# Performance work log

Measured on AMD Instinct MI355X. Metric: run time of the kernel, lower is better.

The kernel has to match this reference:

```python
import jax, jax.numpy as jnp
import numpy as np

NEG = jnp.float32(-1e30)  # safe stand-in for -inf in log-space

def setup_inputs() -> dict:
    key = jax.random.key(0)
    k1, k2, k3, k4 = jax.random.split(key, 4)
    N, C, T, S = 64, 64, 4000, 100
    logits = jax.random.normal(k1, (N, C, T), dtype=jnp.float32)
    targets = jax.random.randint(k2, (N, S), 1, C)          # labels, no blank
    target_lengths = jax.random.randint(k3, (N,), 1, S + 1)  # >= 1
    input_lengths = jax.random.randint(k4, (N,), 2000, T + 1)
    return {"logits": logits, "targets": targets,
            "target_lengths": target_lengths, "input_lengths": input_lengths}

def _lse2(a, b):
    m = jnp.maximum(a, b)
    return m + jnp.log(jnp.exp(a - m) + jnp.exp(b - m))

def _lse3(a, b, c):
    m = jnp.maximum(jnp.maximum(a, b), c)
    return m + jnp.log(jnp.exp(a - m) + jnp.exp(b - m) + jnp.exp(c - m))

def reference(logits, targets, target_lengths, input_lengths):
    # logits: (N, C, T); blank = 0; reduction = 'mean' (per-sample / target_len, then mean)
    N, C, T = logits.shape
    S = targets.shape[1]
    L = 2 * S + 1
    lp = jax.nn.log_softmax(logits, axis=1)      # (N, C, T)
    lp = jnp.transpose(lp, (2, 0, 1))            # (T, N, C)

    # extended label sequence: blank, t1, blank, t2, ..., blank  -> (N, L)
    ext = jnp.zeros((N, L), dtype=targets.dtype).at[:, 1::2].set(targets)
    # skip transition s-2 -> s allowed iff ext[s] != blank and ext[s] != ext[s-2]
    prev2 = jnp.pad(ext[:, :-2], ((0, 0), (2, 0)), constant_values=0)
    skip_ok = (ext != 0) & (ext != prev2)        # (N, L)

    # per-time log-probs of extended labels: (T, N, L)
    lp_ext = jnp.take_along_axis(lp, jnp.broadcast_to(ext[None], (T, N, L)), axis=2)

    # alpha init at t=0
    alpha = jnp.full((N, L), NEG, dtype=lp.dtype)
    alpha = alpha.at[:, 0].set(lp_ext[0, :, 0])
    alpha = alpha.at[:, 1].set(lp_ext[0, :, 1])

    neg1 = jnp.full((N, 1), NEG, dtype=lp.dtype)
    neg2 = jnp.full((N, 2), NEG, dtype=lp.dtype)

    def step(a, inp):
        lpt, t = inp                              # lpt: (N, L)
        a1 = a
        a2 = jnp.concatenate([neg1, a[:, :-1]], axis=1)
        a3 = jnp.concatenate([neg2, a[:, :-2]], axis=1)
        a3 = jnp.where(skip_ok, a3, NEG)
        new = _lse3(a1, a2, a3) + lpt
        active = (t < input_lengths)[:, None]     # freeze past input length
        return jnp.where(active, new, a), None

    alpha, _ = jax.lax.scan(step, alpha, (lp_ext[1:], jnp.arange(1, T)))

    i1 = (2 * target_lengths)[:, None]            # last blank
    i2 = jnp.maximum(i1 - 1, 0)                   # last label
    v1 = jnp.take_along_axis(alpha, i1, axis=1)[:, 0]
    v2 = jnp.take_along_axis(alpha, i2, axis=1)[:, 0]
    loss_n = -_lse2(v1, v2)                       # (N,)
    return jnp.mean(loss_n / target_lengths.astype(loss_n.dtype))
```

## Files before the change

kernel.cpp:

```cpp
#include <hip/hip_runtime.h>
#include <cstdint>
#include <cstddef>

#define NEGV (-1e30f)
#define IL2f 1.44269504088896340736f
#define LN2f 0.693147180559945309417f

__device__ __forceinline__ float exp2_hw(float x) { return __builtin_amdgcn_exp2f(x); }
__device__ __forceinline__ float log2_hw(float x) { return __builtin_amdgcn_logf(x); }

constexpr int Nn = 64, Cc = 64, Tt = 4000, Ss = 100;

__device__ __forceinline__ float wave_shr1(float x) {
    return __int_as_float(__builtin_amdgcn_update_dpp(0, __float_as_int(x), 0x138, 0xF, 0xF, true));
}
__device__ __forceinline__ float wave_shl1(float x) {
    return __int_as_float(__builtin_amdgcn_update_dpp(0, __float_as_int(x), 0x130, 0xF, 0xF, true));
}
__device__ __forceinline__ int wave_shr1_i(int x) {
    return __builtin_amdgcn_update_dpp(0, x, 0x138, 0xF, 0xF, true);
}
__device__ __forceinline__ int wave_shl1_i(int x) {
    return __builtin_amdgcn_update_dpp(0, x, 0x130, 0xF, 0xF, true);
}

typedef float f4 __attribute__((ext_vector_type(4)));
typedef float f2 __attribute__((ext_vector_type(2)));
#define LD4(p) (*(const f4*)(p))

__device__ __forceinline__ void gload16(const float* g, float* l) {
    __builtin_amdgcn_global_load_lds(
        (const __attribute__((address_space(1))) void*)g,
        (__attribute__((address_space(3))) void*)l, 16, 0, 0);
}

__global__ __launch_bounds__(256) void ctc_denom_part(
    const float* __restrict__ logits, float* __restrict__ dP)
{
    const int t4 = (blockIdx.x * 256 + threadIdx.x) * 4;
    const int n = blockIdx.y;
    const int c0 = blockIdx.z * 32;
    if (t4 >= Tt) return;
    const float* __restrict__ p = logits + ((size_t)(n * Cc + c0)) * Tt + t4;
    f4 m, s;
    {
        f4 v = LD4(p);
        #pragma unroll
        for (int i = 0; i < 4; ++i) { m[i] = v[i] * IL2f; s[i] = 1.f; }
    }
    #pragma unroll 4
    for (int c = 1; c < 32; ++c) {
        f4 v = LD4(p + (size_t)c * Tt);
        #pragma unroll
        for (int i = 0; i < 4; ++i) {
            float vi = v[i] * IL2f;
            float nm = fmaxf(m[i], vi);
            s[i] = s[i] * exp2_hw(m[i] - nm) + exp2_hw(vi - nm);
            m[i] = nm;
        }
    }
    f4 o;
    #pragma unroll
    for (int i = 0; i < 4; ++i) o[i] = m[i] + log2_hw(s[i]);
    *(f4*)(dP + ((size_t)blockIdx.z * Nn + n) * Tt + t4) = o;
}

__global__ __launch_bounds__(256) void ctc_denom_kernel(
    const float* __restrict__ logits, float* __restrict__ d2)
{
    const int t4 = (blockIdx.x * 256 + threadIdx.x) * 4;
    const int n = blockIdx.y;
    if (t4 >= Tt) return;
    const float* __restrict__ p = logits + (size_t)n * Cc * Tt + t4;
    f4 m, s;
    {
        f4 v = LD4(p);
        #pragma unroll
        for (int i = 0; i < 4; ++i) { m[i] = v[i] * IL2f; s[i] = 1.f; }
    }
    #pragma unroll 4
    for (int c = 1; c < Cc; ++c) {
        f4 v = LD4(p + (size_t)c * Tt);
        #pragma unroll
        for (int i = 0; i < 4; ++i) {
            float vi = v[i] * IL2f;
            float nm = fmaxf(m[i], vi);
            s[i] = s[i] * exp2_hw(m[i] - nm) + exp2_hw(vi - nm);
            m[i] = nm;
        }
    }
    f4 o;
    #pragma unroll
    for (int i = 0; i < 4; ++i) o[i] = m[i] + log2_hw(s[i]);
    *(f4*)(d2 + (size_t)n * Tt + t4) = o;
}

__global__ __launch_bounds__(256) void ctc_denom_merge(float* __restrict__ dP)
{
    const int t4 = (blockIdx.x * 256 + threadIdx.x) * 4;
    const int n = blockIdx.y;
    if (t4 >= Tt) return;
    f4 a = LD4(dP + (size_t)n * Tt + t4);
    f4 b = LD4(dP + ((size_t)Nn + n) * Tt + t4);
    f4 d;
    #pragma unroll
    for (int i = 0; i < 4; ++i) {
        const float mm = fmaxf(a[i], b[i]);
        d[i] = mm + log2_hw(exp2_hw(a[i] - mm) + exp2_hw(b[i] - mm));
    }
    *(f4*)(dP + (size_t)n * Tt + t4) = d;
}

template<bool MERGE>
__global__ __launch_bounds__(256) void ctc_prob_sel(
    const float* __restrict__ logits, const float* __restrict__ dP,
    const int* __restrict__ targets, const int* __restrict__ tlen,
    float* __restrict__ P)
{
    const int n = blockIdx.y;
    const int c0 = blockIdx.z * 8;
    __shared__ int needs;
    if (threadIdx.x == 0) needs = (c0 == 0) ? 1 : 0;
    __syncthreads();
    const int tl = tlen[n];
    if ((int)threadIdx.x < min(tl, Ss)) {
        const int rel = targets[n * Ss + threadIdx.x] - c0;
        if (rel >= 0 && rel < 8) atomicOr(&needs, 1 << rel);
    }
    __syncthreads();
    const int nd = needs;
    if (nd == 0) return;
    const int t4 = (blockIdx.x * 256 + threadIdx.x) * 4;
    if (t4 >= Tt) return;
    f4 d;
    if constexpr (MERGE) {
        f4 a = LD4(dP + (size_t)n * Tt + t4);
        f4 b = LD4(dP + ((size_t)Nn + n) * Tt + t4);
        #pragma unroll
        for (int i = 0; i < 4; ++i) {
            const float mm = fmaxf(a[i], b[i]);
            d[i] = mm + log2_hw(exp2_hw(a[i] - mm) + exp2_hw(b[i] - mm));
        }
    } else {
        d = LD4(dP + (size_t)n * Tt + t4);
    }
    const float* __restrict__ src = logits + ((size_t)(n * Cc + c0)) * Tt + t4;
    float* __restrict__ dst = P + ((size_t)(n * Cc + c0)) * Tt + t4;
    #pragma unroll
    for (int c = 0; c < 8; ++c) {
        if ((nd >> c) & 1) {
            f4 v = LD4(src + (size_t)c * Tt);
            f4 o;
            #pragma unroll
            for (int i = 0; i < 4; ++i) o[i] = exp2_hw(fmaf(v[i], IL2f, -d[i]));
            *(f4*)(dst + (size_t)c * Tt) = o;
        }
    }
}

template<bool PRE>
__global__ __launch_bounds__(64) void ctc_fb_kernel(
    const float* __restrict__ PR, const int* __restrict__ targets,
    const int* __restrict__ tlen, const int* __restrict__ ilen,
    const float* __restrict__ d2, float* __restrict__ wsA, float* __restrict__ wsB)
{
    constexpr int NA = PRE ? 3 : 4;
    constexpr int NLD = NA * 8;
    __shared__ float lds[2][NA][8][64][4];

    const int bid = blockIdx.x;
    const int n = bid >> 1;
    const bool bwd = bid & 1;
    const int lane = threadIdx.x;
    const int tl = tlen[n];
    const int Tn = ilen[n];
    const int L = 2 * tl + 1;
    const int mid = Tn >> 1;
    const int s0 = 4 * lane;

    const int j1 = min(2 * lane, Ss - 1);
    const int j3 = min(2 * lane + 1, Ss - 1);
    const int base = n * Ss;
    const int tg1 = targets[base + j1];
    const int tg3 = targets[base + j3];
    const int tg1m = targets[base + max(2 * lane - 1, 0)];
    const int tg3p = targets[base + min(2 * lane + 2, Ss - 1)];

    const float sk1f = ((s0 + 1 >= 3) && (tg1 != tg1m)) ? 1.f : 0.f;
    const float sk3f = (tg3 != tg1) ? 1.f : 0.f;
    const float sk1b = ((s0 + 3 < L) && (tg3 != tg1)) ? 1.f : 0.f;
    const float sk3b = ((s0 + 5 < L) && (tg3p != tg3)) ? 1.f : 0.f;

    const float* __restrict__ rB = PR + (size_t)(n * Cc) * Tt;
    const float* __restrict__ r1 = PR + (size_t)(n * Cc + tg1) * Tt;
    const float* __restrict__ r3 = PR + (size_t)(n * Cc + tg3) * Tt;
    const float* __restrict__ rD = d2 + (size_t)n * Tt;

    float a0, a1, a2, a3;
    int E = 0;

    if (!bwd) {
        float pB0, p10;
        if constexpr (PRE) { pB0 = rB[0]; p10 = r1[0]; }
        else {
            const float dv = rD[0];
            pB0 = exp2_hw(fmaf(rB[0], IL2f, -dv));
            p10 = exp2_hw(fmaf(r1[0], IL2f, -dv));
        }
        a0 = (lane == 0) ? pB0 : 0.f;
        a1 = (lane == 0) ? p10 : 0.f;
        a2 = 0.f; a3 = 0.f;
    } else {
        const int te = Tn - 1;
        float pBe, p1e, p3e;
        if constexpr (PRE) { pBe = rB[te]; p1e = r1[te]; p3e = r3[te]; }
        else {
            const float dv = rD[te];
            pBe = exp2_hw(fmaf(rB[te], IL2f, -dv));
            p1e = exp2_hw(fmaf(r1[te], IL2f, -dv));
            p3e = exp2_hw(fmaf(r3[te], IL2f, -dv));
        }
        const int sl = 2 * tl;
        a0 = (s0 == sl) ? pBe : 0.f;
        a1 = (s0 + 1 == sl - 1) ? p1e : 0.f;
        a2 = (s0 + 2 == sl) ? pBe : 0.f;
        a3 = (s0 + 3 == sl - 1) ? p3e : 0.f;
    }

    #define ISSUE(gg, sl) {                                                         \
        const int bo_ = (gg) * 32;                                                  \
        _Pragma("unroll")                                                           \
        for (int j = 0; j < 8; ++j) {                                               \
            gload16(rB + bo_ + 4 * j, &lds[sl][0][j][0][0]);                        \
            gload16(r1 + bo_ + 4 * j, &lds[sl][1][j][0][0]);                        \
            gload16(r3 + bo_ + 4 * j, &lds[sl][2][j][0][0]);                        \
            if constexpr (!PRE) gload16(rD + bo_ + 4 * j, &lds[sl][NA - 1][j][0][0]); \
        }                                                                           \
    }
    #define WAITG() asm volatile("s_waitcnt vmcnt(%0)" :: "n"(NLD) : "memory")
    #define LOADREGS(slc)                                                           \
        f4 vB[8], vU[8], vW[8], vD[8];                                              \
        _Pragma("unroll")                                                           \
        for (int j = 0; j < 8; ++j) {                                               \
            vB[j] = LD4(&lds[slc][0][j][lane][0]);                                  \
            vU[j] = LD4(&lds[slc][1][j][lane][0]);                                  \
            vW[j] = LD4(&lds[slc][2][j][lane][0]);                                  \
            if constexpr (!PRE) vD[j] = LD4(&lds[slc][NA - 1][j][lane][0]);         \
        }                                                                           \
        (void)vD;

    #define RENORM_S(nb) {                                                          \
        const float mx = fmaxf(fmaxf(a0, a1), fmaxf(a2, a3));                       \
        const int me = (int)(__float_as_uint(mx) >> 23);                            \
        const float s2 = __int_as_float((unsigned)(254 - me) << 23);                \
        a0 *= s2; a1 *= s2; a2 *= s2; a3 *= s2;                                     \
        E = (mx > 0.f) ? (E + me - 127) : (nb);                                     \
    }

    if (!bwd) {
        const int tB = mid;
        const int gHi = tB >> 5;

        #define BODY_F_G(gg) {                                                      \
            _Pragma("unroll")                                                       \
            for (int w = 0; w < 4; ++w) {                                           \
                const int Eu = wave_shr1_i(E);                                      \
                const int eb = min(max(127 + (Eu - E), 0), 230);                    \
                const float sc = __int_as_float((unsigned)eb << 23);                \
                const float sk1fs = sk1f * sc;                                      \
                _Pragma("unroll")                                                   \
                for (int kk = 0; kk < 8; ++kk) {                                    \
                    const int k = w * 8 + kk;                                       \
                    const int t = (gg) * 32 + k;                                    \
                    if (t >= 1 && t <= tB) {                                        \
                        float pB, p1, p3;                                           \
                        if constexpr (PRE) {                                        \
                            pB = vB[k >> 2][k & 3]; p1 = vU[k >> 2][k & 3];         \
                            p3 = vW[k >> 2][k & 3];                                 \
                        } else {                                                    \
                            const float dv = vD[k >> 2][k & 3];                     \
                            pB = exp2_hw(fmaf(vB[k >> 2][k & 3], IL2f, -dv));       \
                            p1 = exp2_hw(fmaf(vU[k >> 2][k & 3], IL2f, -dv));       \
                            p3 = exp2_hw(fmaf(vW[k >> 2][k & 3], IL2f, -dv));       \
                        }                                                           \
                        const float u3 = wave_shr1(a3);                             \
                        const float n3 = fmaf(a1, sk3f, a3 + a2) * p3;              \
                        const float n2 = (a2 + a1) * pB;                            \
                        const float n1 = fmaf(u3, sk1fs, a1 + a0) * p1;             \
                        const float n0 = fmaf(u3, sc, a0) * pB;                     \
                        a0 = n0; a1 = n1; a2 = n2; a3 = n3;                         \
                    }                                                               \
                }                                                                   \
                RENORM_S(Eu);                                                       \
            }                                                                       \
        }

        #define BODY_F_F() {                                                        \
            f2 Q0 = {a0, a2}, Q1 = {a1, a3};                                        \
            _Pragma("unroll")                                                       \
            for (int w = 0; w < 4; ++w) {                                           \
                const int Eu = wave_shr1_i(E);                                      \
                const int eb = min(max(127 + (Eu - E), 0), 230);                    \
                const float sc = __int_as_float((unsigned)eb << 23);                \
                const f2 Ksk = {sk3f, sk1f * sc};                                   \
                const f2 K1s = {1.0f, sc};                                          \
                _Pragma("unroll")                                                   \
                for (int kk = 0; kk < 8; ++kk) {                                    \
                    const int k = w * 8 + kk;                                       \
                    const float pB = vB[k >> 2][k & 3];                             \
                    const f2 P31 = {vW[k >> 2][k & 3], vU[k >> 2][k & 3]};          \
                    const f2 PBB = {pB, pB};                                        \
                    const float u3 = wave_shr1(Q1.y);                               \
                    const f2 M = {Q1.x, u3};                                        \
                    const f2 Q0s = __builtin_shufflevector(Q0, Q0, 1, 0);           \
                    const f2 S = __builtin_shufflevector(Q1, Q1, 1, 0) + Q0s;       \
                    const f2 F = __builtin_elementwise_fma(M, Ksk, S);              \
                    const f2 G = __builtin_elementwise_fma(M, K1s, Q0s);            \
                    const f2 N31 = F * P31;                                         \
                    const f2 N20 = G * PBB;                                         \
                    Q1 = __builtin_shufflevector(N31, N31, 1, 0);                   \
                    Q0 = __builtin_shufflevector(N20, N20, 1, 0);                   \
                }                                                                   \
                const f2 mxv = __builtin_elementwise_max(Q0, Q1);                   \
                const float mx = fmaxf(mxv.x, mxv.y);                               \
                const int me = (int)(__float_as_uint(mx) >> 23);                    \
                const float s2 = __int_as_float((unsigned)(254 - me) << 23);        \
                const f2 S2 = {s2, s2};                                             \
                Q0 *= S2; Q1 *= S2;                                                 \
                E = (mx > 0.f) ? (E + me - 127) : Eu;                               \
            }                                                                       \
            a0 = Q0.x; a2 = Q0.y; a1 = Q1.x; a3 = Q1.y;                             \
        }

        ISSUE(0, 0);
        int cur = 0;
        for (int g = 0; g <= gHi; ++g) {
            ISSUE(min(g + 1, gHi), cur ^ 1);
            WAITG();
            LOADREGS(cur);
            cur ^= 1;
            if (PRE && g >= 1 && g * 32 + 31 <= tB) { BODY_F_F(); }
            else                                    { BODY_F_G(g); }
        }
        #undef BODY_F_G
        #undef BODY_F_F
    } else {
        const int tB = Tn - 2, tA = mid + 1;
        const int gHi = tB >> 5, gLo = tA >> 5;

        #define BODY_B_G(gg) {                                                      \
            _Pragma("unroll")                                                       \
            for (int w = 3; w >= 0; --w) {                                          \
                const int Ed = wave_shl1_i(E);                                      \
                const int eb = min(max(127 + (Ed - E), 0), 230);                    \
                const float sc = __int_as_float((unsigned)eb << 23);                \
                const float sk3bs = sk3b * sc;                                      \
                _Pragma("unroll")                                                   \
                for (int kk = 7; kk >= 0; --kk) {                                   \
                    const int k = w * 8 + kk;                                       \
                    const int t = (gg) * 32 + k;                                    \
                    if (t >= tA && t <= tB) {                                       \
                        float pB, p1, p3;                                           \
                        if constexpr (PRE) {                                        \
                            pB = vB[k >> 2][k & 3]; p1 = vU[k >> 2][k & 3];         \
                            p3 = vW[k >> 2][k & 3];                                 \
                        } else {                                                    \
                            const float dv = vD[k >> 2][k & 3];                     \
                            pB = exp2_hw(fmaf(vB[k >> 2][k & 3], IL2f, -dv));       \
                            p1 = exp2_hw(fmaf(vU[k >> 2][k & 3], IL2f, -dv));       \
                            p3 = exp2_hw(fmaf(vW[k >> 2][k & 3], IL2f, -dv));       \
                        }                                                           \
                        const float d0 = wave_shl1(a0);                             \
                        const float d1 = wave_shl1(a1);                             \
                        const float n0 = (a0 + a1) * pB;                            \
                        const float n1 = fmaf(a3, sk1b, a1 + a2) * p1;              \
                        const float n2 = (a2 + a3) * pB;                            \
                        const float n3 = fmaf(d1, sk3bs, fmaf(d0, sc, a3)) * p3;    \
                        a0 = n0; a1 = n1; a2 = n2; a3 = n3;                         \
                    }                                                               \
                }                                                                   \
                RENORM_S(Ed);                                                       \
            }                                                                       \
        }

        #define BODY_B_F() {                                                        \
            f2 Q0 = {a0, a2}, Q1 = {a1, a3};                                        \
            _Pragma("unroll")                                                       \
            for (int w = 3; w >= 0; --w) {                                          \
                const int Ed = wave_shl1_i(E);                                      \
                const int eb = min(max(127 + (Ed - E), 0), 230);                    \
                const float sc = __int_as_float((unsigned)eb << 23);                \
                const f2 K1s = {1.0f, sc};                                          \
                const f2 Ksk = {sk1b, sk3b * sc};                                   \
                _Pragma("unroll")                                                   \
                for (int kk = 7; kk >= 0; --kk) {                                   \
                    const int k = w * 8 + kk;                                       \
                    const float pB = vB[k >> 2][k & 3];                             \
                    const f2 P13 = {vU[k >> 2][k & 3], vW[k >> 2][k & 3]};          \
                    const f2 PBB = {pB, pB};                                        \
                    const float d0 = wave_shl1(Q0.x);                               \
                    const float d1 = wave_shl1(Q1.x);                               \
                    const f2 S = Q0 + Q1;                                           \
                    const f2 A2 = __builtin_elementwise_fma((f2){Q0.y, d0}, K1s, Q1); \
                    const f2 B2 = __builtin_elementwise_fma((f2){Q1.y, d1}, Ksk, A2); \
                    Q1 = B2 * P13;                                                  \
                    Q0 = S * PBB;                                                   \
                }                                                                   \
                const f2 mxv = __builtin_elementwise_max(Q0, Q1);                   \
                const float mx = fmaxf(mxv.x, mxv.y);                               \
                const int me = (int)(__float_as_uint(mx) >> 23);                    \
                const float s2 = __int_as_float((unsigned)(254 - me) << 23);        \
                const f2 S2 = {s2, s2};                                             \
                Q0 *= S2; Q1 *= S2;                                                 \
                E = (mx > 0.f) ? (E + me - 127) : Ed;                               \
            }                                                                       \
            a0 = Q0.x; a2 = Q0.y; a1 = Q1.x; a3 = Q1.y;                             \
        }

        ISSUE(gHi, 0);
        int cur = 0;
        for (int g = gHi; g >= gLo; --g) {
            ISSUE(max(g - 1, 0), cur ^ 1);
            WAITG();
            LOADREGS(cur);
            cur ^= 1;
            if (PRE && g * 32 >= tA && g * 32 + 31 <= tB) { BODY_B_F(); }
            else                                          { BODY_B_G(g); }
        }
        #undef BODY_B_G
        #undef BODY_B_F
    }
    #undef ISSUE
    #undef WAITG
    #undef LOADREGS
    #undef RENORM_S

    float* dst = (bwd ? wsB : wsA) + n * 256;
    const float Ef = (float)E;
    f4 o;
    o[0] = (s0     < L && a0 > 0.f) ? log2_hw(a0) + Ef : NEGV;
    o[1] = (s0 + 1 < L && a1 > 0.f) ? log2_hw(a1) + Ef : NEGV;
    o[2] = (s0 + 2 < L && a2 > 0.f) ? log2_hw(a2) + Ef : NEGV;
    o[3] = (s0 + 3 < L && a3 > 0.f) ? log2_hw(a3) + Ef : NEGV;
    *(f4*)(dst + s0) = o;
}

__global__ __launch_bounds__(64) void ctc_combine_kernel(
    const float* __restrict__ wsA, const float* __restrict__ wsB,
    const int* __restrict__ targets, const int* __restrict__ tlen,
    float* __restrict__ out)
{
    const int n = blockIdx.x;
    const int lane = threadIdx.x;
    const int tl = tlen[n];
    const int L = 2 * tl + 1;
    float vals[4];
    float vmax = NEGV;
    #pragma unroll
    for (int k = 0; k < 4; ++k) {
        const int s = lane + (k << 6);
        float v = NEGV;
        if (s < L) {
            const float al = wsA[n * 256 + s];
            const float b0 = wsB[n * 256 + s];
            const float b1 = (s + 1 < L) ? wsB[n * 256 + s + 1] : NEGV;
            const bool skip = (s & 1) && (s + 2 < L) &&
                (targets[n * Ss + (s >> 1) + 1] != targets[n * Ss + (s >> 1)]);
            const float b2 = skip ? wsB[n * 256 + s + 2] : NEGV;
            const float m3 = fmaxf(fmaxf(b0, b1), b2);
            const float B = m3 + log2_hw(exp2_hw(b0 - m3) + exp2_hw(b1 - m3) + exp2_hw(b2 - m3));
            v = al + B;
        }
        vals[k] = v;
        vmax = fmaxf(vmax, v);
    }
    #pragma unroll
    for (int o = 32; o; o >>= 1) vmax = fmaxf(vmax, __shfl_xor(vmax, o));
    float ssum = 0.f;
    #pragma unroll
    for (int k = 0; k < 4; ++k) ssum += exp2_hw(vals[k] - vmax);
    #pragma unroll
    for (int o = 32; o; o >>= 1) ssum += __shfl_xor(ssum, o);
    if (lane == 0) {
        const float total2 = vmax + log2_hw(ssum);
        const float loss = -LN2f * total2;
        atomicAdd(out, loss / ((float)tl * (float)Nn));
    }
}

extern "C" void kernel_launch(void* const* d_in, const int* in_sizes, int n_in,
                              void* d_out, int out_size, void* d_ws, size_t ws_size,
                              hipStream_t stream) {
    const float* logits = (const float*)d_in[0];
    const int* targets  = (const int*)d_in[1];
    const int* tlen     = (const int*)d_in[2];
    const int* ilen     = (const int*)d_in[3];
    float* out = (float*)d_out;

    float* wsA = (float*)d_ws;
    float* wsB = wsA + Nn * 256;
    float* dP  = wsB + Nn * 256;
    float* P1  = dP + (size_t)2 * Nn * Tt;
    float* P2  = dP + (size_t)Nn * Tt;

    const size_t base = (size_t)Nn * 512;
    const size_t need1 = (base + (size_t)2 * Nn * Tt + (size_t)Nn * Cc * Tt) * 4;
    const size_t need2 = (base + (size_t)Nn * Tt + (size_t)Nn * Cc * Tt) * 4;

    hipMemsetAsync(d_out, 0, sizeof(float), stream);
    if (ws_size >= need1) {
        ctc_denom_part<<<dim3(4, Nn, 2), 256, 0, stream>>>(logits, dP);
        ctc_prob_sel<true><<<dim3(4, Nn, 8), 256, 0, stream>>>(logits, dP, targets, tlen, P1);
        ctc_fb_kernel<true><<<Nn * 2, 64, 0, stream>>>(P1, targets, tlen, ilen, dP, wsA, wsB);
    } else if (ws_size >= need2) {
        ctc_denom_kernel<<<dim3(4, Nn), 256, 0, stream>>>(logits, dP);
        ctc_prob_sel<false><<<dim3(4, Nn, 8), 256, 0, stream>>>(logits, dP, targets, tlen, P2);
        ctc_fb_kernel<true><<<Nn * 2, 64, 0, stream>>>(P2, targets, tlen, ilen, dP, wsA, wsB);
    } else {
        ctc_denom_part<<<dim3(4, Nn, 2), 256, 0, stream>>>(logits, dP);
        ctc_denom_merge<<<dim3(4, Nn), 256, 0, stream>>>(dP);
        ctc_fb_kernel<false><<<Nn * 2, 64, 0, stream>>>(logits, targets, tlen, ilen, dP, wsA, wsB);
    }
    ctc_combine_kernel<<<Nn, 64, 0, stream>>>(wsA, wsB, targets, tlen, out);
}
```

Baseline: 107.8 us.

## Split denominator into four channel chunks, shift fwd/bwd midpoint, drop shuffles

The log-softmax denominator pre-pass now splits channels into four chunks of 16 instead of two of 32. This doubles the grid for better occupancy, and downstream kernels merge four partials instead of two. The forward/backward meeting point moves from half of the input length to 55%, rebalancing work between the forward and backward waves. The forward fast-path body stores the alpha pairs in swapped order, which removes the per-step vector shuffles. The cost is more partial-buffer traffic, extra merge arithmetic, and a larger workspace requirement.

```diff
diff --git a/kernel.cpp b/kernel.cpp
--- a/kernel.cpp
+++ b/kernel.cpp
@@ -34,12 +34,12 @@
         (__attribute__((address_space(3))) void*)l, 16, 0, 0);
 }
 
-__global__ __launch_bounds__(256) void ctc_denom_part(
+__global__ __launch_bounds__(256) void ctc_denom_part4(
     const float* __restrict__ logits, float* __restrict__ dP)
 {
     const int t4 = (blockIdx.x * 256 + threadIdx.x) * 4;
     const int n = blockIdx.y;
-    const int c0 = blockIdx.z * 32;
+    const int c0 = blockIdx.z * 16;
     if (t4 >= Tt) return;
     const float* __restrict__ p = logits + ((size_t)(n * Cc + c0)) * Tt + t4;
     f4 m, s;
@@ -49,7 +49,7 @@
         for (int i = 0; i < 4; ++i) { m[i] = v[i] * IL2f; s[i] = 1.f; }
     }
     #pragma unroll 4
-    for (int c = 1; c < 32; ++c) {
+    for (int c = 1; c < 16; ++c) {
         f4 v = LD4(p + (size_t)c * Tt);
         #pragma unroll
         for (int i = 0; i < 4; ++i) {
@@ -95,23 +95,26 @@
     *(f4*)(d2 + (size_t)n * Tt + t4) = o;
 }
 
-__global__ __launch_bounds__(256) void ctc_denom_merge(float* __restrict__ dP)
+__global__ __launch_bounds__(256) void ctc_denom_merge4(float* __restrict__ dP)
 {
     const int t4 = (blockIdx.x * 256 + threadIdx.x) * 4;
     const int n = blockIdx.y;
     if (t4 >= Tt) return;
     f4 a = LD4(dP + (size_t)n * Tt + t4);
     f4 b = LD4(dP + ((size_t)Nn + n) * Tt + t4);
+    f4 c = LD4(dP + ((size_t)2 * Nn + n) * Tt + t4);
+    f4 e = LD4(dP + ((size_t)3 * Nn + n) * Tt + t4);
     f4 d;
     #pragma unroll
     for (int i = 0; i < 4; ++i) {
-        const float mm = fmaxf(a[i], b[i]);
-        d[i] = mm + log2_hw(exp2_hw(a[i] - mm) + exp2_hw(b[i] - mm));
+        const float mm = fmaxf(fmaxf(a[i], b[i]), fmaxf(c[i], e[i]));
+        d[i] = mm + log2_hw(exp2_hw(a[i] - mm) + exp2_hw(b[i] - mm) +
+                            exp2_hw(c[i] - mm) + exp2_hw(e[i] - mm));
     }
     *(f4*)(dP + (size_t)n * Tt + t4) = d;
 }
 
-template<bool MERGE>
+template<bool MERGE4>
 __global__ __launch_bounds__(256) void ctc_prob_sel(
     const float* __restrict__ logits, const float* __restrict__ dP,
     const int* __restrict__ targets, const int* __restrict__ tlen,
@@ -133,13 +136,16 @@
     const int t4 = (blockIdx.x * 256 + threadIdx.x) * 4;
     if (t4 >= Tt) return;
     f4 d;
-    if constexpr (MERGE) {
+    if constexpr (MERGE4) {
         f4 a = LD4(dP + (size_t)n * Tt + t4);
         f4 b = LD4(dP + ((size_t)Nn + n) * Tt + t4);
+        f4 c = LD4(dP + ((size_t)2 * Nn + n) * Tt + t4);
+        f4 e = LD4(dP + ((size_t)3 * Nn + n) * Tt + t4);
         #pragma unroll
         for (int i = 0; i < 4; ++i) {
-            const float mm = fmaxf(a[i], b[i]);
-            d[i] = mm + log2_hw(exp2_hw(a[i] - mm) + exp2_hw(b[i] - mm));
+            const float mm = fmaxf(fmaxf(a[i], b[i]), fmaxf(c[i], e[i]));
+            d[i] = mm + log2_hw(exp2_hw(a[i] - mm) + exp2_hw(b[i] - mm) +
+                                exp2_hw(c[i] - mm) + exp2_hw(e[i] - mm));
         }
     } else {
         d = LD4(dP + (size_t)n * Tt + t4);
@@ -175,7 +181,7 @@
     const int tl = tlen[n];
     const int Tn = ilen[n];
     const int L = 2 * tl + 1;
-    const int mid = Tn >> 1;
+    const int mid = (int)(((long long)Tn * 11) / 20);
     const int s0 = 4 * lane;
 
     const int j1 = min(2 * lane, Ss - 1);
@@ -296,7 +302,7 @@
         }
 
         #define BODY_F_F() {                                                        \
-            f2 Q0 = {a0, a2}, Q1 = {a1, a3};                                        \
+            f2 Q0 = {a2, a0}, Q1 = {a3, a1};                                        \
             _Pragma("unroll")                                                       \
             for (int w = 0; w < 4; ++w) {                                           \
                 const int Eu = wave_shr1_i(E);                                      \
@@ -310,16 +316,13 @@
                     const float pB = vB[k >> 2][k & 3];                             \
                     const f2 P31 = {vW[k >> 2][k & 3], vU[k >> 2][k & 3]};          \
                     const f2 PBB = {pB, pB};                                        \
-                    const float u3 = wave_shr1(Q1.y);                               \
-                    const f2 M = {Q1.x, u3};                                        \
-                    const f2 Q0s = __builtin_shufflevector(Q0, Q0, 1, 0);           \
-                    const f2 S = __builtin_shufflevector(Q1, Q1, 1, 0) + Q0s;       \
+                    const float u3 = wave_shr1(Q1.x);           \
+                    const f2 M = {Q1.y, u3};                          \
+                    const f2 S = Q1 + Q0;                       \
                     const f2 F = __builtin_elementwise_fma(M, Ksk, S);              \
-                    const f2 G = __builtin_elementwise_fma(M, K1s, Q0s);            \
-                    const f2 N31 = F * P31;                                         \
-                    const f2 N20 = G * PBB;                                         \
-                    Q1 = __builtin_shufflevector(N31, N31, 1, 0);                   \
-                    Q0 = __builtin_shufflevector(N20, N20, 1, 0);                   \
+                    const f2 G = __builtin_elementwise_fma(M, K1s, Q0);             \
+                    Q1 = F * P31;                                     \
+                    Q0 = G * PBB;                                     \
                 }                                                                   \
                 const f2 mxv = __builtin_elementwise_max(Q0, Q1);                   \
                 const float mx = fmaxf(mxv.x, mxv.y);                               \
@@ -329,7 +332,7 @@
                 Q0 *= S2; Q1 *= S2;                                                 \
                 E = (mx > 0.f) ? (E + me - 127) : Eu;                               \
             }                                                                       \
-            a0 = Q0.x; a2 = Q0.y; a1 = Q1.x; a3 = Q1.y;                             \
+            a2 = Q0.x; a0 = Q0.y; a3 = Q1.x; a1 = Q1.y;                             \
         }
 
         ISSUE(0, 0);
@@ -500,16 +503,16 @@
     float* wsA = (float*)d_ws;
     float* wsB = wsA + Nn * 256;
     float* dP  = wsB + Nn * 256;
-    float* P1  = dP + (size_t)2 * Nn * Tt;
+    float* P1  = dP + (size_t)4 * Nn * Tt;
     float* P2  = dP + (size_t)Nn * Tt;
 
     const size_t base = (size_t)Nn * 512;
-    const size_t need1 = (base + (size_t)2 * Nn * Tt + (size_t)Nn * Cc * Tt) * 4;
+    const size_t need1 = (base + (size_t)4 * Nn * Tt + (size_t)Nn * Cc * Tt) * 4;
     const size_t need2 = (base + (size_t)Nn * Tt + (size_t)Nn * Cc * Tt) * 4;
 
     hipMemsetAsync(d_out, 0, sizeof(float), stream);
     if (ws_size >= need1) {
-        ctc_denom_part<<<dim3(4, Nn, 2), 256, 0, stream>>>(logits, dP);
+        ctc_denom_part4<<<dim3(4, Nn, 4), 256, 0, stream>>>(logits, dP);
         ctc_prob_sel<true><<<dim3(4, Nn, 8), 256, 0, stream>>>(logits, dP, targets, tlen, P1);
         ctc_fb_kernel<true><<<Nn * 2, 64, 0, stream>>>(P1, targets, tlen, ilen, dP, wsA, wsB);
     } else if (ws_size >= need2) {
@@ -517,8 +520,8 @@
         ctc_prob_sel<false><<<dim3(4, Nn, 8), 256, 0, stream>>>(logits, dP, targets, tlen, P2);
         ctc_fb_kernel<true><<<Nn * 2, 64, 0, stream>>>(P2, targets, tlen, ilen, dP, wsA, wsB);
     } else {
-        ctc_denom_part<<<dim3(4, Nn, 2), 256, 0, stream>>>(logits, dP);
-        ctc_denom_merge<<<dim3(4, Nn), 256, 0, stream>>>(dP);
+        ctc_denom_part4<<<dim3(4, Nn, 4), 256, 0, stream>>>(logits, dP);
+        ctc_denom_merge4<<<dim3(4, Nn), 256, 0, stream>>>(dP);
         ctc_fb_kernel<false><<<Nn * 2, 64, 0, stream>>>(logits, targets, tlen, ilen, dP, wsA, wsB);
     }
     ctc_combine_kernel<<<Nn, 64, 0, stream>>>(wsA, wsB, targets, tlen, out);
```

Result: no change. 106.2 us (median of 2 runs) (-1.5%).
